# Optimization experiments

Hardware: AMD Instinct MI355X
Metric: run time of the kernel (lower is better)

The kernel has to match this reference:

```python
import jax, jax.numpy as jnp
import numpy as np

D_MODEL = 1024
NHEAD = 16
HEAD_DIM = D_MODEL // NHEAD


def setup_inputs() -> dict:
    key = jax.random.key(0)
    ks = jax.random.split(key, 11)
    B, T = 2, 2048
    s = 1.0 / np.sqrt(D_MODEL)
    return {
        "query": jax.random.normal(ks[0], (B, T, D_MODEL), jnp.float32),
        "key": jax.random.normal(ks[1], (B, T, D_MODEL), jnp.float32),
        "value": jax.random.normal(ks[2], (B, T, D_MODEL), jnp.float32),
        "Wq": jax.random.normal(ks[3], (D_MODEL, D_MODEL), jnp.float32) * s,
        "bq": jnp.zeros((D_MODEL,), jnp.float32),
        "Wk": jax.random.normal(ks[4], (D_MODEL, D_MODEL), jnp.float32) * s,
        "bk": jnp.zeros((D_MODEL,), jnp.float32),
        "Wv": jax.random.normal(ks[5], (D_MODEL, D_MODEL), jnp.float32) * s,
        "bv": jnp.zeros((D_MODEL,), jnp.float32),
        "Wo": jax.random.normal(ks[6], (D_MODEL, D_MODEL), jnp.float32) * s,
        "bo": jnp.zeros((D_MODEL,), jnp.float32),
    }


def reference(query, key, value, Wq, bq, Wk, bk, Wv, bv, Wo, bo):
    B, T, _ = query.shape
    scale = HEAD_DIM ** -0.5
    # Linear projections (torch Linear: x @ W.T + b)
    Q = query @ Wq.T + bq
    K = key @ Wk.T + bk
    V = value @ Wv.T + bv
    # [B, H, T, hd]
    Q = Q.reshape(B, T, NHEAD, HEAD_DIM).transpose(0, 2, 1, 3)
    K = K.reshape(B, T, NHEAD, HEAD_DIM).transpose(0, 2, 1, 3)
    V = V.reshape(B, T, NHEAD, HEAD_DIM).transpose(0, 2, 1, 3)
    # Attention scores [B, H, T, T]
    scores = jnp.einsum("bhqd,bhkd->bhqk", Q, K) * scale
    probs = jax.nn.softmax(scores, axis=-1)
    # dropout is identity in eval mode
    out = jnp.einsum("bhqk,bhkd->bhqd", probs, V)
    out = out.transpose(0, 2, 1, 3).reshape(B, T, D_MODEL)
    return out @ Wo.T + bo
```

## Files before the change

kernel.cpp:

```cpp
#include <hip/hip_runtime.h>
#include <stdint.h>

#define LOG2E_OVER_SQRTHD 0.18033688011112042f
#define SM_BIAS 12.0f

typedef unsigned short u16;
typedef _Float16 f16;
typedef __attribute__((ext_vector_type(4))) float f32x4;
typedef __attribute__((ext_vector_type(8))) _Float16 f16x8;

static __device__ __forceinline__ u16 f2h_bits(float f) {
  union { f16 h; u16 u; } v; v.h = (f16)f; return v.u;
}

static __device__ __forceinline__ void g2l16(const void* g, void* l) {
  __builtin_amdgcn_global_load_lds((const __attribute__((address_space(1))) void*)g,
                                   (__attribute__((address_space(3))) void*)l,
                                   16, 0, 0);
}

__global__ __launch_bounds__(256) void pack_all(
    const float* __restrict__ q, const float* __restrict__ k, const float* __restrict__ v,
    const float* __restrict__ wq, const float* __restrict__ wk,
    const float* __restrict__ wv, const float* __restrict__ wo,
    u16* __restrict__ X, u16* __restrict__ W) {
  int flat = blockIdx.x * 256 + threadIdx.x;
  const float* src;
  u16* dst;
  int idx;
  if (flat < 3 * 1048576) {
    int z = flat >> 20;
    idx = flat & 1048575;
    src = (z == 0) ? q : (z == 1) ? k : v;
    dst = X + (size_t)z * 4194304;
  } else {
    int f2 = flat - 3 * 1048576;
    int z = f2 >> 18;
    idx = f2 & 262143;
    src = (z == 0) ? wq : (z == 1) ? wk : (z == 2) ? wv : wo;
    dst = W + (size_t)z * 1048576;
  }
  float4 x = ((const float4*)src)[idx];
  ushort4 o;
  o.x = f2h_bits(x.x); o.y = f2h_bits(x.y); o.z = f2h_bits(x.z); o.w = f2h_bits(x.w);
  *(ushort4*)(dst + (size_t)idx * 4) = o;
}

template <bool OUT_F16>
static __device__ __forceinline__ void gemm_body(
    const u16* __restrict__ A, const u16* __restrict__ W,
    const float* __restrict__ bias, void* __restrict__ C,
    int ldc, bool row_bias, float oscale, int bm, int bn) {
  __shared__ u16 As[2][128 * 32];
  __shared__ u16 Bs[2][128 * 32];
  const int tid = threadIdx.x;
  const int lane = tid & 63;
  const int wave = tid >> 6;
  const int wm = wave >> 1, wn = wave & 1;
  const int quad = lane >> 4, l15 = lane & 15;

  f32x4 acc[4][4] = {};

  const int r0 = tid >> 2;
  const int c0 = (tid & 3) * 8;
  const u16* Ab = A + (size_t)bm * 1024 + (size_t)r0 * 1024 + c0;
  const u16* Wb = W + (size_t)bn * 1024 + (size_t)r0 * 1024 + c0;

  g2l16(Ab, As[0] + tid * 8);
  g2l16(Ab + 64 * 1024, As[0] + (256 + tid) * 8);
  g2l16(Wb, Bs[0] + tid * 8);
  g2l16(Wb + 64 * 1024, Bs[0] + (256 + tid) * 8);
  __syncthreads();

  for (int kt = 0; kt < 32; ++kt) {
    const int p = kt & 1;
    if (kt + 1 < 32) {
      const int kc = (kt + 1) * 32;
      g2l16(Ab + kc, As[p ^ 1] + tid * 8);
      g2l16(Ab + 64 * 1024 + kc, As[p ^ 1] + (256 + tid) * 8);
      g2l16(Wb + kc, Bs[p ^ 1] + tid * 8);
      g2l16(Wb + 64 * 1024 + kc, Bs[p ^ 1] + (256 + tid) * 8);
    }
    f16x8 af[4], bw[4];
#pragma unroll
    for (int mt = 0; mt < 4; ++mt)
      af[mt] = *(const f16x8*)(As[p] + (wm * 64 + mt * 16 + l15) * 32 + quad * 8);
#pragma unroll
    for (int nt = 0; nt < 4; ++nt)
      bw[nt] = *(const f16x8*)(Bs[p] + (wn * 64 + nt * 16 + l15) * 32 + quad * 8);
#pragma unroll
    for (int mt = 0; mt < 4; ++mt)
#pragma unroll
      for (int nt = 0; nt < 4; ++nt)
        acc[mt][nt] = __builtin_amdgcn_mfma_f32_16x16x32_f16(af[mt], bw[nt], acc[mt][nt], 0, 0, 0);
    __syncthreads();
  }

#pragma unroll
  for (int mt = 0; mt < 4; ++mt) {
    const int row = bm + wm * 64 + mt * 16 + quad * 4;
#pragma unroll
    for (int nt = 0; nt < 4; ++nt) {
      const int col = bn + wn * 64 + nt * 16 + l15;
      const float bcol = row_bias ? 0.0f : bias[col];
#pragma unroll
      for (int i = 0; i < 4; ++i) {
        const float bb = row_bias ? bias[row + i] : bcol;
        float val = (acc[mt][nt][i] + bb) * oscale;
        if (OUT_F16)
          ((u16*)C)[(size_t)(row + i) * ldc + col] = f2h_bits(val);
        else
          ((float*)C)[(size_t)(row + i) * ldc + col] = val;
      }
    }
  }
}

__global__ __launch_bounds__(256) void gemm_qkv(const u16* __restrict__ X,
    const u16* __restrict__ Wf, const float* __restrict__ bq,
    const float* __restrict__ bk, const float* __restrict__ bv,
    u16* __restrict__ QK, u16* __restrict__ Vt, float qscale) {
  const int z = blockIdx.z;
  if (z == 0) {
    gemm_body<true>(X, Wf, bq, QK, 1024, false, qscale,
                    blockIdx.x * 128, blockIdx.y * 128);
  } else if (z == 1) {
    gemm_body<true>(X + (size_t)4194304, Wf + (size_t)1048576, bk,
                    QK + (size_t)4194304, 1024, false, 1.0f,
                    blockIdx.x * 128, blockIdx.y * 128);
  } else {
    gemm_body<true>(Wf + (size_t)2 * 1048576, X + (size_t)2 * 4194304, bv,
                    Vt, 4096, true, 1.0f,
                    blockIdx.y * 128, blockIdx.x * 128);
  }
}

__global__ __launch_bounds__(256) void gemm_out(const u16* __restrict__ O,
    const u16* __restrict__ Wo, const float* __restrict__ bo,
    float* __restrict__ out) {
  gemm_body<false>(O, Wo, bo, out, 1024, false, 1.0f,
                   blockIdx.x * 128, blockIdx.y * 128);
}

__global__ __launch_bounds__(256) void attn_kernel(const u16* __restrict__ QK,
                                                   const u16* __restrict__ Vt,
                                                   u16* __restrict__ O) {
  constexpr int LSP = 68;
  __shared__ u16 Qs[128 * 64];
  __shared__ u16 Ks[64 * 64];
  __shared__ u16 Vts[64 * 64];
  __shared__ u16 Ps[4][32 * LSP];

  const u16* Qb = QK;
  const u16* Kb = QK + (size_t)4096 * 1024;

  const int tid = threadIdx.x, lane = tid & 63, wave = tid >> 6;
  const int quad = lane >> 4, l15 = lane & 15;

  const int id = blockIdx.x;
  const int xcd = id & 7;
  const int j = id >> 3;
  const int qt = j & 15;
  const int hb = xcd + 8 * (j >> 4);
  const int h = hb & 15, b = hb >> 4;

  const size_t qrow0 = (size_t)b * 2048 + qt * 128;
  const size_t kv0 = (size_t)b * 2048;
  const int hc = h * 64;

  const int r0 = tid >> 3;
  const int p0 = tid & 7;
  const int s0 = (p0 ^ (r0 & 7)) * 8;

  g2l16(Qb + (qrow0 + r0) * 1024 + hc + s0, Qs + tid * 8);
  g2l16(Qb + (qrow0 + 32 + r0) * 1024 + hc + s0, Qs + (256 + tid) * 8);
  g2l16(Qb + (qrow0 + 64 + r0) * 1024 + hc + s0, Qs + (512 + tid) * 8);
  g2l16(Qb + (qrow0 + 96 + r0) * 1024 + hc + s0, Qs + (768 + tid) * 8);
  __syncthreads();

  f16x8 aq[2][2];
#pragma unroll
  for (int mt = 0; mt < 2; ++mt) {
    const int Rq = wave * 32 + mt * 16 + l15;
    aq[mt][0] = *(const f16x8*)(Qs + Rq * 64 + ((quad ^ (Rq & 7)) * 8));
    aq[mt][1] = *(const f16x8*)(Qs + Rq * 64 + (((quad + 4) ^ (Rq & 7)) * 8));
  }

  f32x4 o_acc[2][4] = {};
  float l_part[2][4] = {};
  u16* Pw = Ps[wave];

  for (int kt = 0; kt < 32; ++kt) {
    const size_t kr0 = kv0 + (size_t)kt * 64;
    __syncthreads();
    g2l16(Kb + (kr0 + r0) * 1024 + hc + s0, Ks + tid * 8);
    g2l16(Kb + (kr0 + 32 + r0) * 1024 + hc + s0, Ks + (256 + tid) * 8);
    g2l16(Vt + (size_t)(hc + r0) * 4096 + kr0 + s0, Vts + tid * 8);
    g2l16(Vt + (size_t)(hc + 32 + r0) * 4096 + kr0 + s0, Vts + (256 + tid) * 8);
    __syncthreads();

    f32x4 s[2][4];
#pragma unroll
    for (int mt = 0; mt < 2; ++mt)
#pragma unroll
      for (int nt = 0; nt < 4; ++nt)
        s[mt][nt] = f32x4{-SM_BIAS, -SM_BIAS, -SM_BIAS, -SM_BIAS};
#pragma unroll
    for (int nt = 0; nt < 4; ++nt) {
      const int Rk = nt * 16 + l15;
      f16x8 bk0 = *(const f16x8*)(Ks + Rk * 64 + ((quad ^ (Rk & 7)) * 8));
      f16x8 bk1 = *(const f16x8*)(Ks + Rk * 64 + (((quad + 4) ^ (Rk & 7)) * 8));
#pragma unroll
      for (int mt = 0; mt < 2; ++mt) {
        s[mt][nt] = __builtin_amdgcn_mfma_f32_16x16x32_f16(aq[mt][0], bk0, s[mt][nt], 0, 0, 0);
        s[mt][nt] = __builtin_amdgcn_mfma_f32_16x16x32_f16(aq[mt][1], bk1, s[mt][nt], 0, 0, 0);
      }
    }

#pragma unroll
    for (int mt = 0; mt < 2; ++mt)
#pragma unroll
      for (int nt = 0; nt < 4; ++nt)
#pragma unroll
        for (int i = 0; i < 4; ++i) {
          float pe = __builtin_amdgcn_exp2f(s[mt][nt][i]);
          l_part[mt][i] += pe;
          Pw[(mt * 16 + quad * 4 + i) * LSP + nt * 16 + l15] = f2h_bits(pe);
        }
    asm volatile("s_waitcnt lgkmcnt(0)" ::: "memory");

    union U { f16x8 v; struct { uint2 lo, hi; } h; } ap0[2], ap1[2];
#pragma unroll
    for (int mt = 0; mt < 2; ++mt) {
      const u16* Pr = Pw + (mt * 16 + l15) * LSP;
      ap0[mt].h.lo = *(const uint2*)(Pr + quad * 8);
      ap0[mt].h.hi = *(const uint2*)(Pr + quad * 8 + 4);
      ap1[mt].h.lo = *(const uint2*)(Pr + 32 + quad * 8);
      ap1[mt].h.hi = *(const uint2*)(Pr + 32 + quad * 8 + 4);
    }
#pragma unroll
    for (int ct = 0; ct < 4; ++ct) {
      const int Rv = ct * 16 + l15;
      f16x8 bv0 = *(const f16x8*)(Vts + Rv * 64 + ((quad ^ (Rv & 7)) * 8));
      f16x8 bv1 = *(const f16x8*)(Vts + Rv * 64 + (((quad + 4) ^ (Rv & 7)) * 8));
#pragma unroll
      for (int mt = 0; mt < 2; ++mt) {
        o_acc[mt][ct] = __builtin_amdgcn_mfma_f32_16x16x32_f16(ap0[mt].v, bv0, o_acc[mt][ct], 0, 0, 0);
        o_acc[mt][ct] = __builtin_amdgcn_mfma_f32_16x16x32_f16(ap1[mt].v, bv1, o_acc[mt][ct], 0, 0, 0);
      }
    }
  }

#pragma unroll
  for (int mt = 0; mt < 2; ++mt)
#pragma unroll
    for (int i = 0; i < 4; ++i)
#pragma unroll
      for (int d = 1; d < 16; d <<= 1) l_part[mt][i] += __shfl_xor(l_part[mt][i], d);

#pragma unroll
  for (int mt = 0; mt < 2; ++mt)
#pragma unroll
    for (int i = 0; i < 4; ++i) {
      const float inv = 1.0f / l_part[mt][i];
      const size_t row = qrow0 + wave * 32 + mt * 16 + quad * 4 + i;
#pragma unroll
      for (int ct = 0; ct < 4; ++ct) {
        float ov = o_acc[mt][ct][i] * inv;
        int col = hc + ct * 16 + l15;
        O[row * 1024 + col] = f2h_bits(ov);
      }
    }
}

extern "C" void kernel_launch(void* const* d_in, const int* in_sizes, int n_in,
                              void* d_out, int out_size, void* d_ws, size_t ws_size,
                              hipStream_t stream) {
  const float* query = (const float*)d_in[0];
  const float* key   = (const float*)d_in[1];
  const float* value = (const float*)d_in[2];
  const float* Wq = (const float*)d_in[3];
  const float* bq = (const float*)d_in[4];
  const float* Wk = (const float*)d_in[5];
  const float* bk = (const float*)d_in[6];
  const float* Wv = (const float*)d_in[7];
  const float* bv = (const float*)d_in[8];
  const float* Wo = (const float*)d_in[9];
  const float* bo = (const float*)d_in[10];
  float* out = (float*)d_out;

  u16* X  = (u16*)d_ws;
  u16* W  = X + (size_t)3 * 4194304;
  u16* QK = W + (size_t)4 * 1048576;
  u16* Vt = QK + (size_t)2 * 4194304;
  u16* O  = X;

  pack_all<<<dim3(16384, 1, 1), 256, 0, stream>>>(query, key, value, Wq, Wk, Wv, Wo, X, W);
  gemm_qkv<<<dim3(32, 8, 3), 256, 0, stream>>>(X, W, bq, bk, bv, QK, Vt,
                                               LOG2E_OVER_SQRTHD);
  attn_kernel<<<dim3(512, 1, 1), 256, 0, stream>>>(QK, Vt, O);
  gemm_out<<<dim3(32, 8, 1), 256, 0, stream>>>(O, W + (size_t)3 * 1048576, bo, out);
}
```

Before: 238.9 us.

## Use 32x32x16 MFMA in attention with register-resident P via lane shuffles

Rewrites the attention inner loop to compute S^T with 32x32x16 MFMAs so each lane owns one query row. The exp'd probabilities are packed to fp16 and rearranged across half-waves with shuffles instead of a round trip through LDS, which removes the P scratch buffer and the per-lane row-sum reduction. The output is staged through LDS so the global stores are coalesced, and launch bounds now request two blocks per CU. This trades LDS traffic and waits for cross-lane shuffles and higher register pressure per lane.

```diff
diff --git a/kernel.cpp b/kernel.cpp
--- a/kernel.cpp
+++ b/kernel.cpp
@@ -7,10 +7,17 @@
 typedef unsigned short u16;
 typedef _Float16 f16;
 typedef __attribute__((ext_vector_type(4))) float f32x4;
+typedef __attribute__((ext_vector_type(16))) float f32x16;
 typedef __attribute__((ext_vector_type(8))) _Float16 f16x8;
+typedef __attribute__((ext_vector_type(2))) __fp16 fp16x2;
 
 static __device__ __forceinline__ u16 f2h_bits(float f) {
   union { f16 h; u16 u; } v; v.h = (f16)f; return v.u;
+}
+static __device__ __forceinline__ uint32_t pkrtz(float a, float b) {
+  union { fp16x2 h; uint32_t u; } v;
+  v.h = __builtin_amdgcn_cvt_pkrtz(a, b);
+  return v.u;
 }
 
 static __device__ __forceinline__ void g2l16(const void* g, void* l) {
@@ -142,20 +149,18 @@
                    blockIdx.x * 128, blockIdx.y * 128);
 }
 
-__global__ __launch_bounds__(256) void attn_kernel(const u16* __restrict__ QK,
-                                                   const u16* __restrict__ Vt,
-                                                   u16* __restrict__ O) {
-  constexpr int LSP = 68;
-  __shared__ u16 Qs[128 * 64];
+__global__ __launch_bounds__(256, 2) void attn_kernel(const u16* __restrict__ QK,
+                                                      const u16* __restrict__ Vt,
+                                                      u16* __restrict__ O) {
+  __shared__ u16 Qs[128 * 72];
   __shared__ u16 Ks[64 * 64];
   __shared__ u16 Vts[64 * 64];
-  __shared__ u16 Ps[4][32 * LSP];
 
   const u16* Qb = QK;
   const u16* Kb = QK + (size_t)4096 * 1024;
 
   const int tid = threadIdx.x, lane = tid & 63, wave = tid >> 6;
-  const int quad = lane >> 4, l15 = lane & 15;
+  const int q31 = lane & 31, hh = lane >> 5;
 
   const int id = blockIdx.x;
   const int xcd = id & 7;
@@ -178,17 +183,14 @@
   g2l16(Qb + (qrow0 + 96 + r0) * 1024 + hc + s0, Qs + (768 + tid) * 8);
   __syncthreads();
 
-  f16x8 aq[2][2];
-#pragma unroll
-  for (int mt = 0; mt < 2; ++mt) {
-    const int Rq = wave * 32 + mt * 16 + l15;
-    aq[mt][0] = *(const f16x8*)(Qs + Rq * 64 + ((quad ^ (Rq & 7)) * 8));
-    aq[mt][1] = *(const f16x8*)(Qs + Rq * 64 + (((quad + 4) ^ (Rq & 7)) * 8));
-  }
-
-  f32x4 o_acc[2][4] = {};
-  float l_part[2][4] = {};
-  u16* Pw = Ps[wave];
+  f16x8 qf[4];
+  const int Rq = wave * 32 + q31;
+#pragma unroll
+  for (int c = 0; c < 4; ++c)
+    qf[c] = *(const f16x8*)(Qs + Rq * 64 + (((2 * c + hh) ^ (Rq & 7)) * 8));
+
+  f32x16 oacc[2] = {};
+  float l_lane = 0.f;
 
   for (int kt = 0; kt < 32; ++kt) {
     const size_t kr0 = kv0 + (size_t)kt * 64;
@@ -199,78 +201,94 @@
     g2l16(Vt + (size_t)(hc + 32 + r0) * 4096 + kr0 + s0, Vts + (256 + tid) * 8);
     __syncthreads();
 
-    f32x4 s[2][4];
-#pragma unroll
-    for (int mt = 0; mt < 2; ++mt)
-#pragma unroll
-      for (int nt = 0; nt < 4; ++nt)
-        s[mt][nt] = f32x4{-SM_BIAS, -SM_BIAS, -SM_BIAS, -SM_BIAS};
-#pragma unroll
-    for (int nt = 0; nt < 4; ++nt) {
-      const int Rk = nt * 16 + l15;
-      f16x8 bk0 = *(const f16x8*)(Ks + Rk * 64 + ((quad ^ (Rk & 7)) * 8));
-      f16x8 bk1 = *(const f16x8*)(Ks + Rk * 64 + (((quad + 4) ^ (Rk & 7)) * 8));
-#pragma unroll
-      for (int mt = 0; mt < 2; ++mt) {
-        s[mt][nt] = __builtin_amdgcn_mfma_f32_16x16x32_f16(aq[mt][0], bk0, s[mt][nt], 0, 0, 0);
-        s[mt][nt] = __builtin_amdgcn_mfma_f32_16x16x32_f16(aq[mt][1], bk1, s[mt][nt], 0, 0, 0);
+    f32x16 sac[2];
+#pragma unroll
+    for (int t = 0; t < 2; ++t)
+#pragma unroll
+      for (int r = 0; r < 16; ++r) sac[t][r] = -SM_BIAS;
+#pragma unroll
+    for (int t = 0; t < 2; ++t) {
+      const int Rk = t * 32 + q31;
+#pragma unroll
+      for (int c = 0; c < 4; ++c) {
+        f16x8 kf = *(const f16x8*)(Ks + Rk * 64 + (((2 * c + hh) ^ (Rk & 7)) * 8));
+        sac[t] = __builtin_amdgcn_mfma_f32_32x32x16_f16(kf, qf[c], sac[t], 0, 0, 0);
       }
     }
 
-#pragma unroll
-    for (int mt = 0; mt < 2; ++mt)
-#pragma unroll
-      for (int nt = 0; nt < 4; ++nt)
-#pragma unroll
-        for (int i = 0; i < 4; ++i) {
-          float pe = __builtin_amdgcn_exp2f(s[mt][nt][i]);
-          l_part[mt][i] += pe;
-          Pw[(mt * 16 + quad * 4 + i) * LSP + nt * 16 + l15] = f2h_bits(pe);
-        }
-    asm volatile("s_waitcnt lgkmcnt(0)" ::: "memory");
-
-    union U { f16x8 v; struct { uint2 lo, hi; } h; } ap0[2], ap1[2];
-#pragma unroll
-    for (int mt = 0; mt < 2; ++mt) {
-      const u16* Pr = Pw + (mt * 16 + l15) * LSP;
-      ap0[mt].h.lo = *(const uint2*)(Pr + quad * 8);
-      ap0[mt].h.hi = *(const uint2*)(Pr + quad * 8 + 4);
-      ap1[mt].h.lo = *(const uint2*)(Pr + 32 + quad * 8);
-      ap1[mt].h.hi = *(const uint2*)(Pr + 32 + quad * 8 + 4);
-    }
-#pragma unroll
-    for (int ct = 0; ct < 4; ++ct) {
-      const int Rv = ct * 16 + l15;
-      f16x8 bv0 = *(const f16x8*)(Vts + Rv * 64 + ((quad ^ (Rv & 7)) * 8));
-      f16x8 bv1 = *(const f16x8*)(Vts + Rv * 64 + (((quad + 4) ^ (Rv & 7)) * 8));
-#pragma unroll
-      for (int mt = 0; mt < 2; ++mt) {
-        o_acc[mt][ct] = __builtin_amdgcn_mfma_f32_16x16x32_f16(ap0[mt].v, bv0, o_acc[mt][ct], 0, 0, 0);
-        o_acc[mt][ct] = __builtin_amdgcn_mfma_f32_16x16x32_f16(ap1[mt].v, bv1, o_acc[mt][ct], 0, 0, 0);
+    uint32_t dd[2][8];
+#pragma unroll
+    for (int t = 0; t < 2; ++t) {
+      float pe[16];
+#pragma unroll
+      for (int r = 0; r < 16; ++r) pe[r] = __builtin_amdgcn_exp2f(sac[t][r]);
+      float a0 = (pe[0] + pe[1]) + (pe[2] + pe[3]);
+      float a1 = (pe[4] + pe[5]) + (pe[6] + pe[7]);
+      float a2 = (pe[8] + pe[9]) + (pe[10] + pe[11]);
+      float a3 = (pe[12] + pe[13]) + (pe[14] + pe[15]);
+      l_lane += (a0 + a1) + (a2 + a3);
+#pragma unroll
+      for (int k = 0; k < 8; ++k) dd[t][k] = pkrtz(pe[2 * k], pe[2 * k + 1]);
+    }
+
+    uint32_t rp[2][4];
+#pragma unroll
+    for (int t = 0; t < 2; ++t) {
+      uint32_t y0 = hh ? dd[t][0] : dd[t][2];
+      uint32_t y1 = hh ? dd[t][1] : dd[t][3];
+      uint32_t y2 = hh ? dd[t][4] : dd[t][6];
+      uint32_t y3 = hh ? dd[t][5] : dd[t][7];
+      rp[t][0] = (uint32_t)__shfl_xor((int)y0, 32);
+      rp[t][1] = (uint32_t)__shfl_xor((int)y1, 32);
+      rp[t][2] = (uint32_t)__shfl_xor((int)y2, 32);
+      rp[t][3] = (uint32_t)__shfl_xor((int)y3, 32);
+    }
+
+    f16x8 pf[4];
+#pragma unroll
+    for (int t = 0; t < 2; ++t)
+#pragma unroll
+      for (int u = 0; u < 2; ++u) {
+        union { uint32_t w[4]; f16x8 v; } fr;
+        fr.w[0] = hh ? rp[t][2 * u]     : dd[t][4 * u];
+        fr.w[1] = hh ? rp[t][2 * u + 1] : dd[t][4 * u + 1];
+        fr.w[2] = hh ? dd[t][4 * u + 2] : rp[t][2 * u];
+        fr.w[3] = hh ? dd[t][4 * u + 3] : rp[t][2 * u + 1];
+        pf[2 * t + u] = fr.v;
       }
-    }
-  }
-
-#pragma unroll
-  for (int mt = 0; mt < 2; ++mt)
-#pragma unroll
-    for (int i = 0; i < 4; ++i)
-#pragma unroll
-      for (int d = 1; d < 16; d <<= 1) l_part[mt][i] += __shfl_xor(l_part[mt][i], d);
-
-#pragma unroll
-  for (int mt = 0; mt < 2; ++mt)
-#pragma unroll
-    for (int i = 0; i < 4; ++i) {
-      const float inv = 1.0f / l_part[mt][i];
-      const size_t row = qrow0 + wave * 32 + mt * 16 + quad * 4 + i;
-#pragma unroll
-      for (int ct = 0; ct < 4; ++ct) {
-        float ov = o_acc[mt][ct][i] * inv;
-        int col = hc + ct * 16 + l15;
-        O[row * 1024 + col] = f2h_bits(ov);
+
+#pragma unroll
+    for (int dt2 = 0; dt2 < 2; ++dt2) {
+      const int Rv = dt2 * 32 + q31;
+#pragma unroll
+      for (int ch = 0; ch < 4; ++ch) {
+        f16x8 vf = *(const f16x8*)(Vts + Rv * 64 + (((2 * ch + hh) ^ (Rv & 7)) * 8));
+        oacc[dt2] = __builtin_amdgcn_mfma_f32_32x32x16_f16(vf, pf[ch], oacc[dt2], 0, 0, 0);
       }
     }
+  }
+
+  const float l_full = l_lane + __shfl_xor(l_lane, 32);
+  const float inv = 1.0f / l_full;
+
+  const int orow = wave * 32 + q31;
+#pragma unroll
+  for (int dt2 = 0; dt2 < 2; ++dt2)
+#pragma unroll
+    for (int w = 0; w < 8; ++w) {
+      float va = oacc[dt2][2 * w] * inv;
+      float vb = oacc[dt2][2 * w + 1] * inv;
+      uint32_t pk2 = (uint32_t)f2h_bits(va) | ((uint32_t)f2h_bits(vb) << 16);
+      const int dbase = dt2 * 32 + 4 * hh + 8 * (w >> 1) + 2 * (w & 1);
+      *(uint32_t*)(Qs + orow * 72 + dbase) = pk2;
+    }
+  __syncthreads();
+  const int row2 = tid >> 1, c2 = (tid & 1) * 32;
+#pragma unroll
+  for (int k = 0; k < 4; ++k) {
+    uint4 v4 = *(const uint4*)(Qs + row2 * 72 + c2 + 8 * k);
+    *(uint4*)(O + (qrow0 + row2) * 1024 + hc + c2 + 8 * k) = v4;
+  }
 }
 
 extern "C" void kernel_launch(void* const* d_in, const int* in_sizes, int n_in,
```

After: 227.7 us. 1.05x faster.
